# Performance work log

Measured on AMD Instinct MI355X. Metric: run time of the kernel, lower is better.

Reference implementation:

```python
import jax, jax.numpy as jnp
import numpy as np


def setup_inputs() -> dict:
    key = jax.random.key(0)
    k1, k2, k3, k4 = jax.random.split(key, 4)
    B, T, D, H = 4, 4096, 1024, 64
    x = jax.random.normal(k1, (B, T, D), dtype=jnp.float32)
    # nn.Linear(n_embd, head_size, bias=False): store as [D, H] so x @ W matches
    scale = 1.0 / np.sqrt(D)
    Wq = jax.random.normal(k2, (D, H), dtype=jnp.float32) * scale
    Wk = jax.random.normal(k3, (D, H), dtype=jnp.float32) * scale
    Wv = jax.random.normal(k4, (D, H), dtype=jnp.float32) * scale
    return {"x": x, "Wq": Wq, "Wk": Wk, "Wv": Wv}


def reference(x, Wq, Wk, Wv):
    B, T, D = x.shape
    q = jnp.einsum('btd,dh->bth', x, Wq)
    k = jnp.einsum('btd,dh->bth', x, Wk)
    v = jnp.einsum('btd,dh->bth', x, Wv)
    # NOTE: original scales by D**-0.5 where D = n_embd (input dim), not head_size
    scores = jnp.einsum('bth,bsh->bts', q, k) * (D ** -0.5)  # [B,T,T]
    causal = jnp.tril(jnp.ones((T, T), dtype=bool))
    scores = jnp.where(causal, scores, -jnp.inf)
    attn = jax.nn.softmax(scores, axis=-1)
    return jnp.einsum('bts,bsh->bth', attn, v)
```

## Files before the change

kernel.cpp:

```cpp
#include <hip/hip_runtime.h>
#include <hip/hip_bf16.h>
#include <math.h>

typedef __attribute__((ext_vector_type(8))) short bf16x8;
typedef __attribute__((ext_vector_type(4))) float f32x4;
typedef __attribute__((ext_vector_type(16))) float f32x16;
typedef __attribute__((ext_vector_type(2))) unsigned uint2v;

#define MFMA16(A, B, C) __builtin_amdgcn_mfma_f32_16x16x32_bf16(A, B, C, 0, 0, 0)
#define MFMA32(A, B, C) __builtin_amdgcn_mfma_f32_32x32x16_bf16(A, B, C, 0, 0, 0)
#define LOG2E 1.44269504f
#define MB 5.7707801f

__device__ __forceinline__ short f2bf(float f) {
  union { __hip_bfloat16 b; short s; } v;
  v.b = __float2bfloat16(f);
  return v.s;
}

__device__ __forceinline__ float bf2f(short s) {
  union { unsigned u; float f; } v;
  v.u = ((unsigned)(unsigned short)s) << 16;
  return v.f;
}

__device__ __forceinline__ bf16x8 cvt8(float4 a, float4 b) {
  bf16x8 r;
  r[0] = f2bf(a.x); r[1] = f2bf(a.y); r[2] = f2bf(a.z); r[3] = f2bf(a.w);
  r[4] = f2bf(b.x); r[5] = f2bf(b.y); r[6] = f2bf(b.z); r[7] = f2bf(b.w);
  return r;
}

__device__ __forceinline__ unsigned cvt_pk(float lo, float hi) {
  unsigned r;
  asm("v_cvt_pk_bf16_f32 %0, %1, %2" : "=v"(r) : "v"(lo), "v"(hi));
  return r;
}

__device__ __forceinline__ void glds16(const void* g, void* l) {
  __builtin_amdgcn_global_load_lds(
      (const __attribute__((address_space(1))) unsigned int*)g,
      (__attribute__((address_space(3))) unsigned int*)l, 16, 0, 0);
}

__device__ __forceinline__ float xhalf_sum(float x) {
  uint2v r = __builtin_amdgcn_permlane32_swap(__float_as_uint(x), __float_as_uint(x),
                                              false, false);
  return __uint_as_float(r[0]) + __uint_as_float(r[1]);
}

__global__ __launch_bounds__(256) void prep_w(const float* __restrict__ Wq,
                                              const float* __restrict__ Wk,
                                              const float* __restrict__ Wv,
                                              short* __restrict__ Wt) {
  __shared__ float ls[64][65];
  const int wsel = blockIdx.x >> 4;
  const int dt = blockIdx.x & 15;
  const float* W = (wsel == 0) ? Wq : ((wsel == 1) ? Wk : Wv);
  const float scale = (wsel == 0) ? (0.03125f * LOG2E) : 1.0f;
  const int d0 = dt * 64;
  const int rr = threadIdx.x >> 4;
  const int cc = threadIdx.x & 15;
#pragma unroll
  for (int p = 0; p < 4; ++p) {
    int d = rr + p * 16;
    float4 v = *(const float4*)(W + (size_t)(d0 + d) * 64 + cc * 4);
    ls[d][cc * 4 + 0] = v.x; ls[d][cc * 4 + 1] = v.y;
    ls[d][cc * 4 + 2] = v.z; ls[d][cc * 4 + 3] = v.w;
  }
  __syncthreads();
#pragma unroll
  for (int p = 0; p < 4; ++p) {
    int h = rr + p * 16;
    short4 o;
    o.x = f2bf(ls[cc * 4 + 0][h] * scale);
    o.y = f2bf(ls[cc * 4 + 1][h] * scale);
    o.z = f2bf(ls[cc * 4 + 2][h] * scale);
    o.w = f2bf(ls[cc * 4 + 3][h] * scale);
    *(short4*)(Wt + (size_t)(wsel * 64 + h) * 1024 + d0 + cc * 4) = o;
  }
}

__global__ __launch_bounds__(256, 2) void qkv_kernel(const float* __restrict__ x,
                                                     const short* __restrict__ Wt,
                                                     short* __restrict__ qo,
                                                     short* __restrict__ ko,
                                                     short* __restrict__ vT) {
  __shared__ __align__(16) char pool[65536];
  const int tid = threadIdx.x;
  const int wave = tid >> 6, lane = tid & 63;
  const int lr = lane & 15, lq = lane >> 4;
  const int m0 = blockIdx.x * 32;

  f32x4 acc[2][3];
#pragma unroll
  for (int mi = 0; mi < 2; ++mi)
#pragma unroll
    for (int j = 0; j < 3; ++j) acc[mi][j] = f32x4{0.f, 0.f, 0.f, 0.f};

  const int xrow0 = wave * 4 + (lane >> 4);
  const int col16 = lane & 15;
  const float* xg[2];
#pragma unroll
  for (int r = 0; r < 2; ++r) {
    int row = xrow0 + r * 16;
    xg[r] = x + (size_t)(m0 + row) * 1024 + ((col16 ^ (row & 7)) << 2);
  }
  const int wswz = ((lane & 7) ^ (lane >> 3)) << 3;
  const short* wg[6];
#pragma unroll
  for (int r = 0; r < 6; ++r) {
    int n = wave * 8 + (lane >> 3) + r * 32;
    wg[r] = Wt + (size_t)n * 1024 + wswz;
  }
  const int xdst = wave * 1024;
  const int wdst = 8192 + wave * 1024;

#define STAGEQ(c, t)                                                        \
  {                                                                         \
    char* pb = pool + (c) * 32768;                                          \
    glds16(xg[0] + (t) * 64, pb + xdst);                                    \
    glds16(xg[1] + (t) * 64, pb + xdst + 4096);                             \
    _Pragma("unroll") for (int r = 0; r < 6; ++r)                           \
        glds16(wg[r] + (t) * 64, pb + wdst + r * 4096);                     \
  }

  STAGEQ(0, 0)
  __syncthreads();

  int cur = 0;
  for (int t = 0; t < 16; ++t) {
    if (t < 15) STAGEQ(cur ^ 1, t + 1)
    const char* xb = pool + cur * 32768;
    const char* wb = xb + 8192;
#pragma unroll
    for (int kc = 0; kc < 2; ++kc) {
      bf16x8 bfg[3];
#pragma unroll
      for (int j = 0; j < 3; ++j) {
        int n = (wave * 3 + j) * 16 + lr;
        int unit = kc * 4 + lq;
        bfg[j] = *(const bf16x8*)(wb + n * 128 + ((unit ^ (n & 7)) << 4));
      }
#pragma unroll
      for (int mi = 0; mi < 2; ++mi) {
        int row = mi * 16 + lr;
        int p = kc * 4 + lq;
        const char* xr = xb + row * 256;
        float4 a0 = *(const float4*)(xr + (((2 * p) ^ (row & 7)) << 4));
        float4 a1 = *(const float4*)(xr + (((2 * p + 1) ^ (row & 7)) << 4));
        bf16x8 af = cvt8(a0, a1);
#pragma unroll
        for (int j = 0; j < 3; ++j) acc[mi][j] = MFMA16(af, bfg[j], acc[mi][j]);
      }
    }
    __syncthreads();
    cur ^= 1;
  }
#undef STAGEQ

  short* els = (short*)pool;
#pragma unroll
  for (int j = 0; j < 3; ++j) {
    int nt = wave * 3 + j;
#pragma unroll
    for (int mi = 0; mi < 2; ++mi) {
      if (nt < 8) {
#pragma unroll
        for (int r = 0; r < 4; ++r) {
          int mloc = mi * 16 + lq * 4 + r;
          els[mloc * 136 + nt * 16 + lr] = f2bf(acc[mi][j][r]);
        }
      } else {
        int m = m0 + mi * 16 + lq * 4;
        short4 h;
        h.x = f2bf(acc[mi][j][0]); h.y = f2bf(acc[mi][j][1]);
        h.z = f2bf(acc[mi][j][2]); h.w = f2bf(acc[mi][j][3]);
        *(short4*)(vT + ((m >> 12) << 18) + ((nt * 16 + lr - 128) << 12) +
                   (m & 4095)) = h;
      }
    }
  }
  __syncthreads();
  {
    const int m = tid >> 3, nq = tid & 7;
    bf16x8 vq = *(const bf16x8*)(els + m * 136 + nq * 8);
    bf16x8 vk = *(const bf16x8*)(els + m * 136 + 64 + nq * 8);
    *(bf16x8*)(qo + (size_t)(m0 + m) * 64 + nq * 8) = vq;
    *(bf16x8*)(ko + (size_t)(m0 + m) * 64 + nq * 8) = vk;
  }
}

__global__ __launch_bounds__(256) void attn_partial(const short* __restrict__ qbuf,
                                                    const short* __restrict__ kbuf,
                                                    const short* __restrict__ vbuf,
                                                    short* __restrict__ Op,
                                                    float* __restrict__ lp) {
  __shared__ __align__(16) char kv_lds[3][16384];
  const int id = blockIdx.x;
  const int b = id & 3;
  const int u = id >> 2;
  int qt = 0, base = 0;
  while (u >= base + (qt >> 1) + 1) { base += (qt >> 1) + 1; ++qt; }
  const int seg = u - base;
  const int kv_lo = seg << 8;
  const int kv_hi = (seg == (qt >> 1)) ? (qt * 128 + 128) : ((seg + 1) << 8);

  const int tid = threadIdx.x;
  const int wv = tid >> 6, lane = tid & 63;
  const int l31 = lane & 31, hi = lane >> 5;
  const int qr0 = qt * 128 + wv * 32;
  const int qglob = qr0 + l31;

  const short* qb = qbuf + ((size_t)b << 18);
  const short* kb = kbuf + ((size_t)b << 18);
  const short* vb = vbuf + ((size_t)b << 18);

  bf16x8 bq[4];
#pragma unroll
  for (int c = 0; c < 4; ++c)
    bq[c] = *(const bf16x8*)(qb + (size_t)(qr0 + l31) * 64 + c * 16 + hi * 8);

  const int sr = (wv << 4) + (lane >> 3);
  const int swz_s = ((lane & 7) ^ (lane >> 3)) << 3;
  const short* ksrc = kb + (size_t)sr * 64 + swz_s;
  const short* vsrc = vb + (size_t)sr * 4096 + swz_s;
  const int kdst = (wv * 2) * 1024;
  const int vdst = 8192 + (wv * 2) * 1024;

#define STAGE(c, KV0)                                                       \
  {                                                                         \
    char* base_ = kv_lds[c];                                                \
    glds16(ksrc + (size_t)(KV0) * 64, base_ + kdst);                        \
    glds16(ksrc + (size_t)((KV0) + 8) * 64, base_ + kdst + 1024);           \
    glds16(vsrc + (KV0), base_ + vdst);                                     \
    glds16(vsrc + 8 * 4096 + (KV0), base_ + vdst + 1024);                   \
  }

  f32x16 o0, o1;
#pragma unroll
  for (int r = 0; r < 16; ++r) { o0[r] = 0.f; o1[r] = 0.f; }
  float lrow = 0.f;

  union U8 { unsigned u[4]; bf16x8 v; };
  const int swz_r = (l31 & 7);

  STAGE(0, kv_lo)
  if (kv_lo + 64 < kv_hi) STAGE(1, kv_lo + 64)

  int cur = 0;
  for (int kv0 = kv_lo; kv0 < kv_hi; kv0 += 64) {
    const bool h1 = (kv0 + 64 < kv_hi);
    const bool h2 = (kv0 + 128 < kv_hi);
    if (h2) {
      int nb = cur + 2; if (nb >= 3) nb -= 3;
      STAGE(nb, kv0 + 128)
    }
    if (h2)      asm volatile("s_waitcnt vmcnt(8)" ::: "memory");
    else if (h1) asm volatile("s_waitcnt vmcnt(4)" ::: "memory");
    else         asm volatile("s_waitcnt vmcnt(0)" ::: "memory");
    __builtin_amdgcn_s_barrier();

    if (kv0 <= qr0 + 31) {
      const int kv1 = kv0 + 32;
      const char* kl = kv_lds[cur];
      const char* vl = kv_lds[cur] + 8192;
      bf16x8 ka[4], kc[4], va[8];
#pragma unroll
      for (int c = 0; c < 4; ++c) {
        ka[c] = *(const bf16x8*)(kl + l31 * 128 + (((c * 2 + hi) ^ swz_r) << 4));
        kc[c] = *(const bf16x8*)(kl + (32 + l31) * 128 + (((c * 2 + hi) ^ swz_r) << 4));
      }
#pragma unroll
      for (int h = 0; h < 2; ++h)
#pragma unroll
        for (int p = 0; p < 4; ++p)
          va[h * 4 + p] = *(const bf16x8*)(vl + (32 * h + l31) * 128 +
                                           (((2 * p + hi) ^ swz_r) << 4));

      f32x16 s0, s1;
#pragma unroll
      for (int r = 0; r < 16; ++r) { s0[r] = 0.f; s1[r] = 0.f; }
#pragma unroll
      for (int c = 0; c < 4; ++c) {
        s0 = MFMA32(ka[c], bq[c], s0);
        s1 = MFMA32(kc[c], bq[c], s1);
      }

      if (kv0 + 31 > qr0) {
#pragma unroll
        for (int r = 0; r < 16; ++r)
          if (kv0 + (r & 3) + 8 * (r >> 2) + 4 * hi > qglob) s0[r] = -1e30f;
      }
      if (kv1 + 31 > qr0) {
#pragma unroll
        for (int r = 0; r < 16; ++r)
          if (kv1 + (r & 3) + 8 * (r >> 2) + 4 * hi > qglob) s1[r] = -1e30f;
      }

      float p0[16], p1[16];
#pragma unroll
      for (int r = 0; r < 16; ++r) {
        p0[r] = exp2f(s0[r] - MB);
        p1[r] = exp2f(s1[r] - MB);
      }
      float a8[8];
#pragma unroll
      for (int r = 0; r < 8; ++r) a8[r] = (p0[r] + p0[r + 8]) + (p1[r] + p1[r + 8]);
      float s4 = ((a8[0] + a8[4]) + (a8[1] + a8[5])) +
                 ((a8[2] + a8[6]) + (a8[3] + a8[7]));
      lrow += xhalf_sum(s4);

#define MAKE_FRAGS(P, UA, UB)                                                  \
      {                                                                        \
        unsigned c0 = cvt_pk(P[0], P[1]), c1 = cvt_pk(P[2], P[3]);             \
        unsigned c2 = cvt_pk(P[4], P[5]), c3 = cvt_pk(P[6], P[7]);             \
        unsigned c4 = cvt_pk(P[8], P[9]), c5 = cvt_pk(P[10], P[11]);           \
        unsigned c6 = cvt_pk(P[12], P[13]), c7 = cvt_pk(P[14], P[15]);         \
        uint2v rA = __builtin_amdgcn_permlane32_swap(c0, c2, false, false);    \
        uint2v rB = __builtin_amdgcn_permlane32_swap(c1, c3, false, false);    \
        uint2v rC = __builtin_amdgcn_permlane32_swap(c4, c6, false, false);    \
        uint2v rD = __builtin_amdgcn_permlane32_swap(c5, c7, false, false);    \
        UA.u[0] = rA[0]; UA.u[2] = rA[1];                                      \
        UA.u[1] = rB[0]; UA.u[3] = rB[1];                                      \
        UB.u[0] = rC[0]; UB.u[2] = rC[1];                                      \
        UB.u[1] = rD[0]; UB.u[3] = rD[1];                                      \
      }
      U8 pa00, pa01, pa10, pa11;
      MAKE_FRAGS(p0, pa00, pa01)
      MAKE_FRAGS(p1, pa10, pa11)
#undef MAKE_FRAGS

      o0 = MFMA32(va[0], pa00.v, o0);
      o0 = MFMA32(va[1], pa01.v, o0);
      o0 = MFMA32(va[2], pa10.v, o0);
      o0 = MFMA32(va[3], pa11.v, o0);
      o1 = MFMA32(va[4], pa00.v, o1);
      o1 = MFMA32(va[5], pa01.v, o1);
      o1 = MFMA32(va[6], pa10.v, o1);
      o1 = MFMA32(va[7], pa11.v, o1);
    }

    __builtin_amdgcn_s_barrier();
    cur = (cur == 2) ? 0 : cur + 1;
  }
#undef STAGE

  const int pid = b * 272 + u;
  short* Ob = Op + (size_t)pid * 8192;
#pragma unroll
  for (int r = 0; r < 16; ++r) {
    int hd = (r & 3) + 8 * (r >> 2) + 4 * hi;
    Ob[hd * 128 + wv * 32 + l31] = f2bf(o0[r]);
    Ob[(32 + hd) * 128 + wv * 32 + l31] = f2bf(o1[r]);
  }
  if (hi == 0) lp[pid * 128 + wv * 32 + l31] = lrow;
}

__global__ __launch_bounds__(256) void attn_combine(const short* __restrict__ Op,
                                                    const float* __restrict__ lp,
                                                    float* __restrict__ out) {
  __shared__ float ls[32][128];
  const int qt = blockIdx.x;
  const int b = blockIdx.y;
  const int zh = blockIdx.z;
  const int m = qt >> 1, e = qt & 1;
  const int nseg = m + 1;
  const int base = b * 272 + qt + m * (m - 1) + e * m;

  const int qc = threadIdx.x & 127, hh = threadIdx.x >> 7;
  float lsum = 0.f;
  for (int s = 0; s < nseg; ++s) lsum += lp[(base + s) * 128 + qc];
  const float inv = 1.0f / lsum;

  float osum[16];
#pragma unroll
  for (int i = 0; i < 16; ++i) osum[i] = 0.f;
  for (int s = 0; s < nseg; ++s) {
    const short* Ob = Op + (size_t)(base + s) * 8192;
#pragma unroll
    for (int i = 0; i < 16; ++i)
      osum[i] += bf2f(Ob[(zh * 32 + hh * 16 + i) * 128 + qc]);
  }
#pragma unroll
  for (int i = 0; i < 16; ++i) ls[hh * 16 + i][qc] = osum[i] * inv;
  __syncthreads();

  const int row = threadIdx.x >> 1, ch = (threadIdx.x & 1) * 16;
  float4 w4[4];
#pragma unroll
  for (int g4 = 0; g4 < 4; ++g4) {
    w4[g4].x = ls[ch + g4 * 4 + 0][row];
    w4[g4].y = ls[ch + g4 * 4 + 1][row];
    w4[g4].z = ls[ch + g4 * 4 + 2][row];
    w4[g4].w = ls[ch + g4 * 4 + 3][row];
  }
  float* op = out + ((size_t)b * 4096 + (size_t)qt * 128 + row) * 64 + zh * 32 + ch;
#pragma unroll
  for (int g4 = 0; g4 < 4; ++g4) *(float4*)(op + g4 * 4) = w4[g4];
}

extern "C" void kernel_launch(void* const* d_in, const int* in_sizes, int n_in,
                              void* d_out, int out_size, void* d_ws, size_t ws_size,
                              hipStream_t stream) {
  const float* x = (const float*)d_in[0];
  const float* Wq = (const float*)d_in[1];
  const float* Wk = (const float*)d_in[2];
  const float* Wv = (const float*)d_in[3];
  float* out = (float*)d_out;

  char* w = (char*)d_ws;
  short* qb = (short*)(w);
  short* kb = (short*)(w + (size_t)2 * 1024 * 1024);
  short* vT = (short*)(w + (size_t)4 * 1024 * 1024);
  short* Wt = (short*)(w + (size_t)6 * 1024 * 1024);
  float* lp = (float*)(w + (size_t)6656 * 1024);
  short* Op = (short*)(w + (size_t)7424 * 1024);

  prep_w<<<48, 256, 0, stream>>>(Wq, Wk, Wv, Wt);
  qkv_kernel<<<512, 256, 0, stream>>>(x, Wt, qb, kb, vT);
  attn_partial<<<1088, 256, 0, stream>>>(qb, kb, vT, Op, lp);
  attn_combine<<<dim3(32, 4, 2), 256, 0, stream>>>(Op, lp, out);
}
```

Baseline: 69.33 us.

## Fuse split-KV combine into attention kernel via last-arriver atomic counter

Drops the separate combine launch. Each partial attention block now fences its writes and increments a per-(batch, q-tile) atomic counter. The last block to finish a q-tile reduces all segment partials and writes the final normalized output. The counters are zeroed in the weight-prep kernel. This saves one kernel launch and its tail gap, but the finishing block does serialized combine work (both head halves) at the end of the attention kernel and adds atomics and fences.

```diff
diff --git a/kernel.cpp b/kernel.cpp
--- a/kernel.cpp
+++ b/kernel.cpp
@@ -52,8 +52,10 @@
 __global__ __launch_bounds__(256) void prep_w(const float* __restrict__ Wq,
                                               const float* __restrict__ Wk,
                                               const float* __restrict__ Wv,
-                                              short* __restrict__ Wt) {
+                                              short* __restrict__ Wt,
+                                              unsigned* __restrict__ cnt) {
   __shared__ float ls[64][65];
+  if (blockIdx.x == 0 && threadIdx.x < 128) cnt[threadIdx.x] = 0u;
   const int wsel = blockIdx.x >> 4;
   const int dt = blockIdx.x & 15;
   const float* W = (wsel == 0) ? Wq : ((wsel == 1) ? Wk : Wv);
@@ -195,7 +197,9 @@
                                                     const short* __restrict__ kbuf,
                                                     const short* __restrict__ vbuf,
                                                     short* __restrict__ Op,
-                                                    float* __restrict__ lp) {
+                                                    float* __restrict__ lp,
+                                                    unsigned* __restrict__ cnt,
+                                                    float* __restrict__ out) {
   __shared__ __align__(16) char kv_lds[3][16384];
   const int id = blockIdx.x;
   const int b = id & 3;
@@ -355,49 +359,53 @@
     Ob[(32 + hd) * 128 + wv * 32 + l31] = f2bf(o1[r]);
   }
   if (hi == 0) lp[pid * 128 + wv * 32 + l31] = lrow;
-}
-
-__global__ __launch_bounds__(256) void attn_combine(const short* __restrict__ Op,
-                                                    const float* __restrict__ lp,
-                                                    float* __restrict__ out) {
-  __shared__ float ls[32][128];
-  const int qt = blockIdx.x;
-  const int b = blockIdx.y;
-  const int zh = blockIdx.z;
-  const int m = qt >> 1, e = qt & 1;
-  const int nseg = m + 1;
-  const int base = b * 272 + qt + m * (m - 1) + e * m;
-
-  const int qc = threadIdx.x & 127, hh = threadIdx.x >> 7;
+
+  __threadfence();
+  __syncthreads();
+  int* flag = (int*)kv_lds[0];
+  if (tid == 0) {
+    unsigned old = atomicAdd(&cnt[b * 32 + qt], 1u);
+    flag[0] = (old == (unsigned)(qt >> 1)) ? 1 : 0;
+  }
+  __syncthreads();
+  if (flag[0] == 0) return;
+  __threadfence();
+
+  const int nseg2 = (qt >> 1) + 1;
+  const int pb0 = b * 272 + (u - seg);
+  const int qc = tid & 127, hh = tid >> 7;
   float lsum = 0.f;
-  for (int s = 0; s < nseg; ++s) lsum += lp[(base + s) * 128 + qc];
+  for (int s2 = 0; s2 < nseg2; ++s2) lsum += lp[(pb0 + s2) * 128 + qc];
   const float inv = 1.0f / lsum;
 
-  float osum[16];
-#pragma unroll
-  for (int i = 0; i < 16; ++i) osum[i] = 0.f;
-  for (int s = 0; s < nseg; ++s) {
-    const short* Ob = Op + (size_t)(base + s) * 8192;
-#pragma unroll
-    for (int i = 0; i < 16; ++i)
-      osum[i] += bf2f(Ob[(zh * 32 + hh * 16 + i) * 128 + qc]);
-  }
-#pragma unroll
-  for (int i = 0; i < 16; ++i) ls[hh * 16 + i][qc] = osum[i] * inv;
-  __syncthreads();
-
-  const int row = threadIdx.x >> 1, ch = (threadIdx.x & 1) * 16;
-  float4 w4[4];
-#pragma unroll
-  for (int g4 = 0; g4 < 4; ++g4) {
-    w4[g4].x = ls[ch + g4 * 4 + 0][row];
-    w4[g4].y = ls[ch + g4 * 4 + 1][row];
-    w4[g4].z = ls[ch + g4 * 4 + 2][row];
-    w4[g4].w = ls[ch + g4 * 4 + 3][row];
-  }
-  float* op = out + ((size_t)b * 4096 + (size_t)qt * 128 + row) * 64 + zh * 32 + ch;
-#pragma unroll
-  for (int g4 = 0; g4 < 4; ++g4) *(float4*)(op + g4 * 4) = w4[g4];
+  float* lsbuf = (float*)(kv_lds[0] + 512);
+  for (int zh = 0; zh < 2; ++zh) {
+    float osum[16];
+#pragma unroll
+    for (int i = 0; i < 16; ++i) osum[i] = 0.f;
+    for (int s2 = 0; s2 < nseg2; ++s2) {
+      const short* Os = Op + (size_t)(pb0 + s2) * 8192;
+#pragma unroll
+      for (int i = 0; i < 16; ++i)
+        osum[i] += bf2f(Os[(zh * 32 + hh * 16 + i) * 128 + qc]);
+    }
+#pragma unroll
+    for (int i = 0; i < 16; ++i) lsbuf[(hh * 16 + i) * 128 + qc] = osum[i] * inv;
+    __syncthreads();
+    const int row = tid >> 1, ch = (tid & 1) * 16;
+    float4 w4[4];
+#pragma unroll
+    for (int g4 = 0; g4 < 4; ++g4) {
+      w4[g4].x = lsbuf[(ch + g4 * 4 + 0) * 128 + row];
+      w4[g4].y = lsbuf[(ch + g4 * 4 + 1) * 128 + row];
+      w4[g4].z = lsbuf[(ch + g4 * 4 + 2) * 128 + row];
+      w4[g4].w = lsbuf[(ch + g4 * 4 + 3) * 128 + row];
+    }
+    float* op = out + ((size_t)b * 4096 + (size_t)qt * 128 + row) * 64 + zh * 32 + ch;
+#pragma unroll
+    for (int g4 = 0; g4 < 4; ++g4) *(float4*)(op + g4 * 4) = w4[g4];
+    __syncthreads();
+  }
 }
 
 extern "C" void kernel_launch(void* const* d_in, const int* in_sizes, int n_in,
@@ -415,10 +423,10 @@
   short* vT = (short*)(w + (size_t)4 * 1024 * 1024);
   short* Wt = (short*)(w + (size_t)6 * 1024 * 1024);
   float* lp = (float*)(w + (size_t)6656 * 1024);
+  unsigned* cnt = (unsigned*)(w + (size_t)7300 * 1024);
   short* Op = (short*)(w + (size_t)7424 * 1024);
 
-  prep_w<<<48, 256, 0, stream>>>(Wq, Wk, Wv, Wt);
+  prep_w<<<48, 256, 0, stream>>>(Wq, Wk, Wv, Wt, cnt);
   qkv_kernel<<<512, 256, 0, stream>>>(x, Wt, qb, kb, vT);
-  attn_partial<<<1088, 256, 0, stream>>>(qb, kb, vT, Op, lp);
-  attn_combine<<<dim3(32, 4, 2), 256, 0, stream>>>(Op, lp, out);
-}
+  attn_partial<<<1088, 256, 0, stream>>>(qb, kb, vT, Op, lp, cnt, out);
+}
```

New measurement: 212.9 us. 207% more time.
